# Performance work log

Hardware: AMD Instinct MI355X
Metric: run time of the kernel (lower is better)

Reference implementation:

```python
import jax, jax.numpy as jnp
import numpy as np

NUM_BINS = 64
Z_MIN, Z_MAX = -3.0, 1.0
BIN_SIZE = (Z_MAX - Z_MIN) / NUM_BINS
EPS_MEAN = 1e-5
EPS_BN = 1e-5


def setup_inputs() -> dict:
    key = jax.random.key(0)
    k1, k2, k3, k4 = jax.random.split(key, 4)
    M, N, C = 100000, 64, 4
    feat_channels, out_dim = 64, NUM_BINS * 3
    features = jax.random.normal(k1, (M, N, C), dtype=jnp.float32)
    num_points = jax.random.randint(k2, (M,), 0, 65, dtype=jnp.int32)
    coors = jax.random.randint(k3, (M, 4), 0, 100, dtype=jnp.int32)
    W = jax.random.normal(k4, (feat_channels, out_dim), dtype=jnp.float32) * (1.0 / np.sqrt(out_dim))
    b = jnp.zeros((feat_channels,), dtype=jnp.float32)
    gamma = jnp.ones((feat_channels,), dtype=jnp.float32)
    beta = jnp.zeros((feat_channels,), dtype=jnp.float32)
    return {"features": features, "num_points": num_points, "coors": coors,
            "W": W, "b": b, "gamma": gamma, "beta": beta}


def reference(features, num_points, coors, W, b, gamma, beta):
    M, N, C = features.shape
    # validity mask per point
    mask = (jnp.arange(N)[None, :] < num_points[:, None]).astype(features.dtype)  # [M, N]
    z = features[..., 2]  # [M, N]
    r = features[..., 3]  # [M, N]
    bin_idx = jnp.clip(((z - Z_MIN) / BIN_SIZE).astype(jnp.int32), 0, NUM_BINS - 1)  # [M, N]

    rows = jnp.arange(M)[:, None]  # [M, 1] broadcast against [M, N]
    zeros = jnp.zeros((M, NUM_BINS), dtype=features.dtype)
    count = zeros.at[rows, bin_idx].add(mask)
    sum_z = zeros.at[rows, bin_idx].add(z * mask)
    sum_r = zeros.at[rows, bin_idx].add(r * mask)
    mean_z = sum_z / (count + EPS_MEAN)
    mean_r = sum_r / (count + EPS_MEAN)

    # interleaved layout [count, mean_z, mean_r] per bin -> [M, 3*NUM_BINS]
    hist = jnp.stack([count, mean_z, mean_r], axis=-1).reshape(M, NUM_BINS * 3)

    # Linear -> BatchNorm1d (training: biased batch stats) -> ReLU
    x = hist @ W.T + b  # [M, feat_channels]
    mu = jnp.mean(x, axis=0)
    var = jnp.mean((x - mu) ** 2, axis=0)
    xn = (x - mu) / jnp.sqrt(var + EPS_BN)
    return jax.nn.relu(xn * gamma + beta)
```

## Files before the change

kernel.cpp:

```cpp
#include <hip/hip_runtime.h>
#include <hip/hip_bf16.h>
#include <math.h>


typedef __attribute__((ext_vector_type(8))) short bf16x8;
typedef __attribute__((ext_vector_type(4))) float f32x4;
typedef __attribute__((ext_vector_type(4))) int   i32x4;

#define ZMINF   (-3.0f)
#define INV_BIN 16.0f
#define HROWS   16
#define HPAD    132
#define QS      8192.0f
#define INV_QS  (1.0f / 8192.0f)
#define PBIASF  65536.0f
#define PBIASI  65536
#define CBIT    16777216
#define TSC     16777216.0f
#define INV_TSC (1.0f / 16777216.0f)
#define REPS    16

__device__ __forceinline__ short f2bf(float f) {
    __hip_bfloat16 h = __float2bfloat16(f);
    return __builtin_bit_cast(short, h);
}

__global__ __launch_bounds__(256)
void k0_prep(const float* __restrict__ W,
             short*       __restrict__ wsW,
             unsigned long long* __restrict__ totals)
{
    const int tid = threadIdx.x;
    for (int e = tid; e < 24 * 64 * 8; e += 256) {
        const int j  = e & 7;
        const int ln = (e >> 3) & 63;
        const int st = e >> 9;
        const int s  = st >> 2, t = st & 3;
        const int k  = s * 32 + (ln >> 4) * 8 + j;
        const int n  = t * 16 + (ln & 15);
        const int wc = (k < 64) ? 3 * k
                     : (k < 128) ? 3 * (k - 64) + 1
                                 : 3 * (k - 128) + 2;
        wsW[e] = f2bf(W[n * 192 + wc]);
    }
    for (int e = tid; e < REPS * 128; e += 256) totals[e] = 0ull;
}

__global__ __launch_bounds__(256, 4)
void k1_hist_mfma(const uint2*  __restrict__ feat2,
                  const int*    __restrict__ nump,
                  const bf16x8* __restrict__ wsWf,
                  const float*  __restrict__ bvec,
                  float*        __restrict__ xout,
                  unsigned long long* __restrict__ totals,
                  int M)
{
    __shared__ int sH[4 * HROWS * HPAD];

    const int tid  = threadIdx.x;
    const int wave = tid >> 6;
    const int lane = tid & 63;
    const int col  = lane & 15;
    const int quad = lane >> 4;

    const int gbase = (blockIdx.x * 4 + wave) * HROWS;
    int* hw = &sH[wave * HROWS * HPAD];
    float psum[4] = {0.f, 0.f, 0.f, 0.f};
    float psq[4]  = {0.f, 0.f, 0.f, 0.f};

    if (gbase < M) {
        uint2 zw[HROWS];
        const int npv = nump[min(gbase + (lane & 15), M - 1)];
        #pragma unroll
        for (int u = 0; u < HROWS; ++u) {
            const int rc = min(gbase + u, M - 1);
            zw[u] = feat2[((size_t)rc * 64 + lane) * 2 + 1];
        }

        {
            i32x4* p4 = (i32x4*)hw;
            #pragma unroll
            for (int i = 0; i < 9; ++i) {
                const int idx = lane + i * 64;
                if (idx < (HROWS * HPAD) / 4) p4[idx] = i32x4{0, 0, 0, 0};
            }
        }
        __builtin_amdgcn_wave_barrier();

        #pragma unroll
        for (int u = 0; u < HROWS; ++u) {
            int np_u = __builtin_amdgcn_readlane(npv, u);
            np_u = (gbase + u < M) ? np_u : 0;
            if (lane < np_u) {
                const float z  = __int_as_float((int)zw[u].x);
                const float rr = __int_as_float((int)zw[u].y);
                int bi = (int)((z - ZMINF) * INV_BIN);
                bi = min(max(bi, 0), 63);
                int* hrow = hw + u * HPAD;
                atomicAdd(hrow + bi,      CBIT + PBIASI + (int)(z * QS));
                atomicAdd(hrow + 64 + bi, PBIASI + (int)(rr * QS));
            }
        }
        __builtin_amdgcn_wave_barrier();
        __threadfence_block();

        f32x4 acc[4] = {};
        bf16x8 bcur[4], bnxt[4];
        #pragma unroll
        for (int t = 0; t < 4; ++t) bcur[t] = wsWf[t * 64 + lane];

        const int* ar = hw + col * HPAD;
        int   z0[8], z1[8];
        float cnt0[8], cnt1[8], rcp0[8], rcp1[8];
        #pragma unroll
        for (int s = 0; s < 6; ++s) {
            if (s < 5) {
                #pragma unroll
                for (int t = 0; t < 4; ++t) bnxt[t] = wsWf[((s + 1) * 4 + t) * 64 + lane];
            }
            float av[8];
            if (s == 0 || s == 1) {
                const i32x4* ap = (const i32x4*)(ar + s * 32 + quad * 8);
                const i32x4 a0 = ap[0], a1 = ap[1];
                int* zc = (s == 0) ? z0 : z1;
                float* cc = (s == 0) ? cnt0 : cnt1;
                zc[0]=a0.x; zc[1]=a0.y; zc[2]=a0.z; zc[3]=a0.w;
                zc[4]=a1.x; zc[5]=a1.y; zc[6]=a1.z; zc[7]=a1.w;
                #pragma unroll
                for (int j = 0; j < 8; ++j) { cc[j] = (float)(zc[j] >> 24); av[j] = cc[j]; }
            } else if (s == 2 || s == 3) {
                const int*   zc = (s == 2) ? z0 : z1;
                const float* cc = (s == 2) ? cnt0 : cnt1;
                float* rp = (s == 2) ? rcp0 : rcp1;
                #pragma unroll
                for (int j = 0; j < 8; ++j) {
                    rp[j] = __builtin_amdgcn_rcpf(cc[j] + 1e-5f) * INV_QS;
                    const float pay = (float)(zc[j] & 0xFFFFFF);
                    av[j] = (pay - cc[j] * PBIASF) * rp[j];
                }
            } else {
                const i32x4* ap = (const i32x4*)(ar + 64 + (s - 4) * 32 + quad * 8);
                const i32x4 a0 = ap[0], a1 = ap[1];
                const int rv[8] = {a0.x, a0.y, a0.z, a0.w, a1.x, a1.y, a1.z, a1.w};
                const float* cc = (s == 4) ? cnt0 : cnt1;
                const float* rp = (s == 4) ? rcp0 : rcp1;
                #pragma unroll
                for (int j = 0; j < 8; ++j)
                    av[j] = ((float)rv[j] - cc[j] * PBIASF) * rp[j];
            }
            bf16x8 af;
            #pragma unroll
            for (int j = 0; j < 8; ++j) af[j] = f2bf(av[j]);
            #pragma unroll
            for (int t = 0; t < 4; ++t)
                acc[t] = __builtin_amdgcn_mfma_f32_16x16x32_bf16(af, bcur[t], acc[t], 0, 0, 0);
            #pragma unroll
            for (int t = 0; t < 4; ++t) bcur[t] = bnxt[t];
        }

        #pragma unroll
        for (int t = 0; t < 4; ++t) {
            const float bias = bvec[t * 16 + col];
            #pragma unroll
            for (int i = 0; i < 4; ++i) {
                const int row = gbase + quad * 4 + i;
                if (row < M) {
                    const float xv = acc[t][i] + bias;
                    xout[(size_t)row * 64 + t * 16 + col] = xv;
                    psum[t] += xv;
                    psq[t]  += xv * xv;
                }
            }
        }
    }

    #pragma unroll
    for (int t = 0; t < 4; ++t) {
        psum[t] += __shfl_xor(psum[t], 16);
        psum[t] += __shfl_xor(psum[t], 32);
        psq[t]  += __shfl_xor(psq[t], 16);
        psq[t]  += __shfl_xor(psq[t], 32);
    }
    float myS = psum[0], myQ = psq[0];
    if (quad == 1) { myS = psum[1]; myQ = psq[1]; }
    if (quad == 2) { myS = psum[2]; myQ = psq[2]; }
    if (quad == 3) { myS = psum[3]; myQ = psq[3]; }
    const int gw = blockIdx.x * 4 + wave;
    unsigned long long* dst = totals + (gw & (REPS - 1)) * 128 + lane;
    atomicAdd(dst,      (unsigned long long)(long long)(myS * TSC));
    atomicAdd(dst + 64, (unsigned long long)(long long)(myQ * TSC));
}

__global__ __launch_bounds__(256)
void k3_bn_apply(float4* __restrict__ x,
                 const unsigned long long* __restrict__ totals,
                 const float* __restrict__ gamma,
                 const float* __restrict__ beta,
                 float invM, int n4)
{
    __shared__ float sT[128];
    __shared__ float sa[64];
    __shared__ float sc[64];
    const int t = threadIdx.x;
    if (t < 128) {
        long long s = 0;
        #pragma unroll
        for (int rep = 0; rep < REPS; ++rep) s += (long long)totals[rep * 128 + t];
        sT[t] = (float)s * (invM * INV_TSC);
    }
    __syncthreads();
    if (t < 64) {
        const float mu   = sT[t];
        const float q    = sT[64 + t];
        const float var  = q - mu * mu;
        const float rstd = 1.0f / sqrtf(var + 1e-5f);
        const float a    = gamma[t] * rstd;
        sa[t] = a;
        sc[t] = beta[t] - mu * a;
    }
    __syncthreads();
    const int stride = gridDim.x * 256;
    for (int i = blockIdx.x * 256 + t; i < n4; i += stride) {
        const float4 a = ((const float4*)sa)[i & 15];
        const float4 c = ((const float4*)sc)[i & 15];
        float4 v = x[i];
        v.x = fmaxf(fmaf(v.x, a.x, c.x), 0.f);
        v.y = fmaxf(fmaf(v.y, a.y, c.y), 0.f);
        v.z = fmaxf(fmaf(v.z, a.z, c.z), 0.f);
        v.w = fmaxf(fmaf(v.w, a.w, c.w), 0.f);
        x[i] = v;
    }
}

extern "C" void kernel_launch(void* const* d_in, const int* in_sizes, int n_in,
                              void* d_out, int out_size, void* d_ws, size_t ws_size,
                              hipStream_t stream) {
    const uint2*  feat2 = (const uint2*)d_in[0];
    const int*    nump  = (const int*)d_in[1];
    const float*  W     = (const float*)d_in[3];
    const float*  bvec  = (const float*)d_in[4];
    const float*  gamma = (const float*)d_in[5];
    const float*  beta  = (const float*)d_in[6];

    const int M = in_sizes[1];
    float* xout = (float*)d_out;
    short* wsW  = (short*)d_ws;
    unsigned long long* totals =
        (unsigned long long*)((char*)d_ws + 24 * 64 * 8 * sizeof(short));

    k0_prep<<<1, 256, 0, stream>>>(W, wsW, totals);

    const int nblk = (M + 4 * HROWS - 1) / (4 * HROWS);
    k1_hist_mfma<<<nblk, 256, 0, stream>>>(feat2, nump, (const bf16x8*)wsW, bvec, xout, totals, M);

    const int n4 = out_size / 4;
    const int nblk3 = (n4 + 256 * 16 - 1) / (256 * 16);
    k3_bn_apply<<<nblk3, 256, 0, stream>>>((float4*)d_out, totals, gamma, beta,
                                           1.0f / (float)M, n4);
}
```

Measured before the change: 203.7 us.

## Split each 16-row histogram tile across two waves with swizzled shared layout

Each pair of waves now shares one 16-row histogram tile. Each wave builds 8 rows, the block synchronizes, and each wave then computes two of the four 16-column output tiles. The shared histogram drops its padding and uses a per-row rotation swizzle to avoid bank conflicts, which halves LDS use and lets launch bounds request 8 blocks per SM. The prep kernel is also spread over 16 blocks. This costs a block-wide barrier in place of wave-local barriers, and each wave now reads the whole tile for its MFMA A operand.

```diff
diff --git a/kernel.cpp b/kernel.cpp
--- a/kernel.cpp
+++ b/kernel.cpp
@@ -9,8 +9,6 @@
 
 #define ZMINF   (-3.0f)
 #define INV_BIN 16.0f
-#define HROWS   16
-#define HPAD    132
 #define QS      8192.0f
 #define INV_QS  (1.0f / 8192.0f)
 #define PBIASF  65536.0f
@@ -30,8 +28,9 @@
              short*       __restrict__ wsW,
              unsigned long long* __restrict__ totals)
 {
-    const int tid = threadIdx.x;
-    for (int e = tid; e < 24 * 64 * 8; e += 256) {
+    const int tid    = blockIdx.x * 256 + threadIdx.x;
+    const int stride = gridDim.x * 256;
+    for (int e = tid; e < 24 * 64 * 8; e += stride) {
         const int j  = e & 7;
         const int ln = (e >> 3) & 63;
         const int st = e >> 9;
@@ -43,10 +42,10 @@
                                  : 3 * (k - 128) + 2;
         wsW[e] = f2bf(W[n * 192 + wc]);
     }
-    for (int e = tid; e < REPS * 128; e += 256) totals[e] = 0ull;
-}
-
-__global__ __launch_bounds__(256, 4)
+    for (int e = tid; e < REPS * 128; e += stride) totals[e] = 0ull;
+}
+
+__global__ __launch_bounds__(256, 8)
 void k1_hist_mfma(const uint2*  __restrict__ feat2,
                   const int*    __restrict__ nump,
                   const bf16x8* __restrict__ wsWf,
@@ -55,73 +54,83 @@
                   unsigned long long* __restrict__ totals,
                   int M)
 {
-    __shared__ int sH[4 * HROWS * HPAD];
+    __shared__ int sH[2 * 16 * 128];
 
     const int tid  = threadIdx.x;
     const int wave = tid >> 6;
     const int lane = tid & 63;
     const int col  = lane & 15;
     const int quad = lane >> 4;
-
-    const int gbase = (blockIdx.x * 4 + wave) * HROWS;
-    int* hw = &sH[wave * HROWS * HPAD];
-    float psum[4] = {0.f, 0.f, 0.f, 0.f};
-    float psq[4]  = {0.f, 0.f, 0.f, 0.f};
+    const int pair = wave >> 1;
+    const int half = wave & 1;
+
+    const int gbase = blockIdx.x * 32 + pair * 16;
+    int* hp = &sH[pair * 2048];
+
+    float psum[2] = {0.f, 0.f};
+    float psq[2]  = {0.f, 0.f};
+    bf16x8 bcur[2];
 
     if (gbase < M) {
-        uint2 zw[HROWS];
-        const int npv = nump[min(gbase + (lane & 15), M - 1)];
-        #pragma unroll
-        for (int u = 0; u < HROWS; ++u) {
-            const int rc = min(gbase + u, M - 1);
-            zw[u] = feat2[((size_t)rc * 64 + lane) * 2 + 1];
+        uint2 zw[8];
+        const int npv = nump[min(gbase + half * 8 + (lane & 7), M - 1)];
+        #pragma unroll
+        for (int uu = 0; uu < 8; ++uu) {
+            const int rc = min(gbase + half * 8 + uu, M - 1);
+            zw[uu] = feat2[((size_t)rc * 64 + lane) * 2 + 1];
         }
 
         {
-            i32x4* p4 = (i32x4*)hw;
-            #pragma unroll
-            for (int i = 0; i < 9; ++i) {
-                const int idx = lane + i * 64;
-                if (idx < (HROWS * HPAD) / 4) p4[idx] = i32x4{0, 0, 0, 0};
-            }
+            i32x4* p4 = (i32x4*)(hp + half * 1024);
+            #pragma unroll
+            for (int i = 0; i < 4; ++i) p4[lane + i * 64] = i32x4{0, 0, 0, 0};
         }
         __builtin_amdgcn_wave_barrier();
 
         #pragma unroll
-        for (int u = 0; u < HROWS; ++u) {
-            int np_u = __builtin_amdgcn_readlane(npv, u);
+        for (int uu = 0; uu < 8; ++uu) {
+            const int u = half * 8 + uu;
+            int np_u = __builtin_amdgcn_readlane(npv, uu);
             np_u = (gbase + u < M) ? np_u : 0;
             if (lane < np_u) {
-                const float z  = __int_as_float((int)zw[u].x);
-                const float rr = __int_as_float((int)zw[u].y);
+                const float z  = __int_as_float((int)zw[uu].x);
+                const float rr = __int_as_float((int)zw[uu].y);
                 int bi = (int)((z - ZMINF) * INV_BIN);
                 bi = min(max(bi, 0), 63);
-                int* hrow = hw + u * HPAD;
-                atomicAdd(hrow + bi,      CBIT + PBIASI + (int)(z * QS));
-                atomicAdd(hrow + 64 + bi, PBIASI + (int)(rr * QS));
-            }
-        }
-        __builtin_amdgcn_wave_barrier();
-        __threadfence_block();
-
-        f32x4 acc[4] = {};
-        bf16x8 bcur[4], bnxt[4];
-        #pragma unroll
-        for (int t = 0; t < 4; ++t) bcur[t] = wsWf[t * 64 + lane];
-
-        const int* ar = hw + col * HPAD;
+                const int sw = (bi + u * 4) & 63;
+                int* hrow = hp + u * 128;
+                atomicAdd(hrow + sw,      CBIT + PBIASI + (int)(z * QS));
+                atomicAdd(hrow + 64 + sw, PBIASI + (int)(rr * QS));
+            }
+        }
+
+        #pragma unroll
+        for (int tt = 0; tt < 2; ++tt)
+            bcur[tt] = wsWf[(half * 2 + tt) * 64 + lane];
+    }
+
+    __syncthreads();
+
+    if (gbase < M) {
+        f32x4 acc[2] = {};
+        bf16x8 bnxt[2];
+        const int* ar  = hp + col * 128;
+        const int  rot = col * 4;
         int   z0[8], z1[8];
         float cnt0[8], cnt1[8], rcp0[8], rcp1[8];
         #pragma unroll
         for (int s = 0; s < 6; ++s) {
             if (s < 5) {
                 #pragma unroll
-                for (int t = 0; t < 4; ++t) bnxt[t] = wsWf[((s + 1) * 4 + t) * 64 + lane];
+                for (int tt = 0; tt < 2; ++tt)
+                    bnxt[tt] = wsWf[((s + 1) * 4 + half * 2 + tt) * 64 + lane];
             }
             float av[8];
             if (s == 0 || s == 1) {
-                const i32x4* ap = (const i32x4*)(ar + s * 32 + quad * 8);
-                const i32x4 a0 = ap[0], a1 = ap[1];
+                const int o0 = (s * 32 + quad * 8 + rot) & 63;
+                const int o1 = (s * 32 + quad * 8 + 4 + rot) & 63;
+                const i32x4 a0 = *(const i32x4*)(ar + o0);
+                const i32x4 a1 = *(const i32x4*)(ar + o1);
                 int* zc = (s == 0) ? z0 : z1;
                 float* cc = (s == 0) ? cnt0 : cnt1;
                 zc[0]=a0.x; zc[1]=a0.y; zc[2]=a0.z; zc[3]=a0.w;
@@ -139,8 +148,10 @@
                     av[j] = (pay - cc[j] * PBIASF) * rp[j];
                 }
             } else {
-                const i32x4* ap = (const i32x4*)(ar + 64 + (s - 4) * 32 + quad * 8);
-                const i32x4 a0 = ap[0], a1 = ap[1];
+                const int o0 = ((s - 4) * 32 + quad * 8 + rot) & 63;
+                const int o1 = ((s - 4) * 32 + quad * 8 + 4 + rot) & 63;
+                const i32x4 a0 = *(const i32x4*)(ar + 64 + o0);
+                const i32x4 a1 = *(const i32x4*)(ar + 64 + o1);
                 const int rv[8] = {a0.x, a0.y, a0.z, a0.w, a1.x, a1.y, a1.z, a1.w};
                 const float* cc = (s == 4) ? cnt0 : cnt1;
                 const float* rp = (s == 4) ? rcp0 : rcp1;
@@ -152,43 +163,44 @@
             #pragma unroll
             for (int j = 0; j < 8; ++j) af[j] = f2bf(av[j]);
             #pragma unroll
-            for (int t = 0; t < 4; ++t)
-                acc[t] = __builtin_amdgcn_mfma_f32_16x16x32_bf16(af, bcur[t], acc[t], 0, 0, 0);
-            #pragma unroll
-            for (int t = 0; t < 4; ++t) bcur[t] = bnxt[t];
-        }
-
-        #pragma unroll
-        for (int t = 0; t < 4; ++t) {
+            for (int tt = 0; tt < 2; ++tt)
+                acc[tt] = __builtin_amdgcn_mfma_f32_16x16x32_bf16(af, bcur[tt], acc[tt], 0, 0, 0);
+            #pragma unroll
+            for (int tt = 0; tt < 2; ++tt) bcur[tt] = bnxt[tt];
+        }
+
+        #pragma unroll
+        for (int tt = 0; tt < 2; ++tt) {
+            const int t = half * 2 + tt;
             const float bias = bvec[t * 16 + col];
             #pragma unroll
             for (int i = 0; i < 4; ++i) {
                 const int row = gbase + quad * 4 + i;
                 if (row < M) {
-                    const float xv = acc[t][i] + bias;
+                    const float xv = acc[tt][i] + bias;
                     xout[(size_t)row * 64 + t * 16 + col] = xv;
-                    psum[t] += xv;
-                    psq[t]  += xv * xv;
+                    psum[tt] += xv;
+                    psq[tt]  += xv * xv;
                 }
             }
         }
     }
 
     #pragma unroll
-    for (int t = 0; t < 4; ++t) {
-        psum[t] += __shfl_xor(psum[t], 16);
-        psum[t] += __shfl_xor(psum[t], 32);
-        psq[t]  += __shfl_xor(psq[t], 16);
-        psq[t]  += __shfl_xor(psq[t], 32);
-    }
-    float myS = psum[0], myQ = psq[0];
-    if (quad == 1) { myS = psum[1]; myQ = psq[1]; }
-    if (quad == 2) { myS = psum[2]; myQ = psq[2]; }
-    if (quad == 3) { myS = psum[3]; myQ = psq[3]; }
+    for (int tt = 0; tt < 2; ++tt) {
+        psum[tt] += __shfl_xor(psum[tt], 16);
+        psum[tt] += __shfl_xor(psum[tt], 32);
+        psq[tt]  += __shfl_xor(psq[tt], 16);
+        psq[tt]  += __shfl_xor(psq[tt], 32);
+    }
+    const float myS = (quad & 1) ? psum[1] : psum[0];
+    const float myQ = (quad & 1) ? psq[1]  : psq[0];
     const int gw = blockIdx.x * 4 + wave;
-    unsigned long long* dst = totals + (gw & (REPS - 1)) * 128 + lane;
-    atomicAdd(dst,      (unsigned long long)(long long)(myS * TSC));
-    atomicAdd(dst + 64, (unsigned long long)(long long)(myQ * TSC));
+    if (lane < 32) {
+        unsigned long long* dst = totals + (gw & (REPS - 1)) * 128 + half * 32 + lane;
+        atomicAdd(dst,      (unsigned long long)(long long)(myS * TSC));
+        atomicAdd(dst + 64, (unsigned long long)(long long)(myQ * TSC));
+    }
 }
 
 __global__ __launch_bounds__(256)
@@ -248,9 +260,9 @@
     unsigned long long* totals =
         (unsigned long long*)((char*)d_ws + 24 * 64 * 8 * sizeof(short));
 
-    k0_prep<<<1, 256, 0, stream>>>(W, wsW, totals);
-
-    const int nblk = (M + 4 * HROWS - 1) / (4 * HROWS);
+    k0_prep<<<16, 256, 0, stream>>>(W, wsW, totals);
+
+    const int nblk = (M + 31) / 32;
     k1_hist_mfma<<<nblk, 256, 0, stream>>>(feat2, nump, (const bf16x8*)wsW, bvec, xout, totals, M);
 
     const int n4 = out_size / 4;
```

New measurement: 193.2 us. 5.2% less time.
